# Kernel tuning notes

Measured on AMD Instinct MI355X. Metric: run time of the kernel, lower is better.

## Reference

```python
import jax, jax.numpy as jnp
import numpy as np

DIM = 768
NUM_HEADS = 12
HEAD_DIM = DIM // NUM_HEADS
H = W = 64
RANK = 4
LORA_SCALING = 1.0 / RANK  # lora_alpha(=1) / r


def setup_inputs() -> dict:
    key = jax.random.key(0)
    ks = jax.random.split(key, 11)
    s = 0.02
    return {
        "x": jax.random.normal(ks[0], (1, H, W, DIM), dtype=jnp.float32),
        "W_qkv": jax.random.normal(ks[1], (3 * DIM, DIM), dtype=jnp.float32) * s,
        "b_qkv": jax.random.normal(ks[2], (3 * DIM,), dtype=jnp.float32) * s,
        "A_q": jax.random.normal(ks[3], (RANK, DIM), dtype=jnp.float32) * s,
        "B_q": jax.random.normal(ks[4], (DIM, RANK), dtype=jnp.float32) * s,
        "A_v": jax.random.normal(ks[5], (RANK, DIM), dtype=jnp.float32) * s,
        "B_v": jax.random.normal(ks[6], (DIM, RANK), dtype=jnp.float32) * s,
        "rel_h": jax.random.normal(ks[7], (2 * H - 1, HEAD_DIM), dtype=jnp.float32) * s,
        "rel_w": jax.random.normal(ks[8], (2 * W - 1, HEAD_DIM), dtype=jnp.float32) * s,
        "W_proj": jax.random.normal(ks[9], (DIM, DIM), dtype=jnp.float32) * s,
        "b_proj": jax.random.normal(ks[10], (DIM,), dtype=jnp.float32) * s,
    }


def _get_rel_pos(size, rel_pos):
    # q_size == k_size == size; relative coords indexed into (2*size-1, head_dim)
    coords = jnp.arange(size)[:, None] - jnp.arange(size)[None, :] + (size - 1)
    return rel_pos[coords]  # (size, size, head_dim)


def reference(x, W_qkv, b_qkv, A_q, B_q, A_v, B_v, rel_h, rel_w, W_proj, b_proj):
    B, h, w, dim = x.shape
    nh, hd = NUM_HEADS, HEAD_DIM
    scale = hd ** -0.5
    n = h * w
    xf = x.reshape(B, n, dim)

    # LoRA-merged QKV: base linear + low-rank deltas on q and v thirds only
    qkv = xf @ W_qkv.T + b_qkv  # (B, n, 3*dim)
    dq = ((xf @ A_q.T) @ B_q.T) * LORA_SCALING
    dv = ((xf @ A_v.T) @ B_v.T) * LORA_SCALING
    qkv = qkv.at[..., :dim].add(dq).at[..., 2 * dim:].add(dv)

    qkv = qkv.reshape(B, n, 3, nh, hd).transpose(2, 0, 3, 1, 4).reshape(3, B * nh, n, hd)
    q, k, v = qkv[0], qkv[1], qkv[2]  # each (B*nh, n, hd)

    attn = (q * scale) @ jnp.swapaxes(k, -2, -1)  # (B*nh, n, n)

    # decomposed relative position bias (SAM style)
    Rh = _get_rel_pos(h, rel_h)  # (h, h, hd)
    Rw = _get_rel_pos(w, rel_w)  # (w, w, hd)
    r_q = q.reshape(B * nh, h, w, hd)
    bias_h = jnp.einsum("bhwc,hkc->bhwk", r_q, Rh)  # (B*nh, h, w, h)
    bias_w = jnp.einsum("bhwc,wkc->bhwk", r_q, Rw)  # (B*nh, h, w, w)
    attn = (attn.reshape(B * nh, h, w, h, w)
            + bias_h[:, :, :, :, None]
            + bias_w[:, :, :, None, :]).reshape(B * nh, n, n)

    attn = jax.nn.softmax(attn, axis=-1)
    out = (attn @ v).reshape(B, nh, h, w, hd).transpose(0, 2, 3, 1, 4).reshape(B, h, w, dim)
    return out @ W_proj.T + b_proj
```

## Files before the change

kernel.cpp:

```cpp
#include <hip/hip_runtime.h>

#define NTOK 4096
#define DIMD 768
#define NHD  12
#define HDD  64
#define DK   800

typedef float  f32x4  __attribute__((ext_vector_type(4)));
typedef float  f32x16 __attribute__((ext_vector_type(16)));
typedef short  s16x8  __attribute__((ext_vector_type(8)));

#define MFMA16(a, b, c) __builtin_amdgcn_mfma_f32_16x16x32_bf16(a, b, c, 0, 0, 0)
#define MFMA32(a, b, c) __builtin_amdgcn_mfma_f32_32x32x16_bf16(a, b, c, 0, 0, 0)

__device__ inline short f2b(float f) {
  unsigned u = __float_as_uint(f);
  u += 0x7FFFu + ((u >> 16) & 1u);
  return (short)(u >> 16);
}
__device__ inline float b2f(short s) {
  return __uint_as_float(((unsigned)(unsigned short)s) << 16);
}
__device__ inline void gl_lds16(const short* g, short* l) {
  __builtin_amdgcn_global_load_lds(
      (const __attribute__((address_space(1))) unsigned int*)g,
      (__attribute__((address_space(3))) unsigned int*)l, 16, 0, 0);
}


__global__ __launch_bounds__(64)
void k_prep_w(const float* __restrict__ Wqkv, const float* __restrict__ Bq,
              const float* __restrict__ Bv, const float* __restrict__ Wp,
              short* __restrict__ we, short* __restrict__ wpb) {
  const int j = blockIdx.x;
  const int l = threadIdx.x;
  if (j < 2304) {
#pragma unroll
    for (int k = 0; k < 12; ++k)
      we[(size_t)j * DK + l + 64 * k] = f2b(Wqkv[(size_t)j * DIMD + l + 64 * k]);
    if (l < 32) {
      int c = 768 + l;
      short v = 0;
      if (l < 4) {
        if (j < 768) v = f2b(Bq[j * 4 + l]);
      } else if (l < 8) {
        if (j >= 1536) v = f2b(Bv[(j - 1536) * 4 + (l - 4)]);
      }
      we[(size_t)j * DK + c] = v;
    }
  } else {
    const int jr = j - 2304;
#pragma unroll
    for (int k = 0; k < 12; ++k)
      wpb[(size_t)jr * DIMD + l + 64 * k] =
          f2b(Wp[(size_t)jr * DIMD + l + 64 * k]);
  }
}

__global__ __launch_bounds__(64)
void k_prep_x(const float* __restrict__ x, const float* __restrict__ Aq,
              const float* __restrict__ Av, short* __restrict__ xe) {
  const int i = blockIdx.x;
  const int l = threadIdx.x;
  float xv[12];
#pragma unroll
  for (int k = 0; k < 12; ++k) xv[k] = x[(size_t)i * DIMD + l + 64 * k];
#pragma unroll
  for (int k = 0; k < 12; ++k)
    xe[(size_t)i * DK + l + 64 * k] = f2b(xv[k]);
  float a8[8];
#pragma unroll
  for (int o = 0; o < 8; ++o) {
    const float* A = (o < 4) ? (Aq + o * DIMD) : (Av + (o - 4) * DIMD);
    float acc = 0.f;
#pragma unroll
    for (int k = 0; k < 12; ++k) acc = fmaf(xv[k], A[l + 64 * k], acc);
#pragma unroll
    for (int off = 32; off; off >>= 1) acc += __shfl_xor(acc, off, 64);
    a8[o] = acc;
  }
  if (l < 32) {
    float v = 0.f;
#pragma unroll
    for (int o = 0; o < 8; ++o)
      if (l == o) v = 0.25f * a8[o];
    xe[(size_t)i * DK + 768 + l] = (l < 8) ? f2b(v) : (short)0;
  }
}

__global__ __launch_bounds__(256)
void k_qkv(const short* __restrict__ xe, const short* __restrict__ we,
           const float* __restrict__ bqkv, short* __restrict__ qkvb) {
  const int j0 = blockIdx.x * 128;
  const int i0 = blockIdx.y * 128;
  __shared__ short As[128 * 32];
  __shared__ short Bs[128 * 32];
  __shared__ short Cs[128 * 130];
  const int t = threadIdx.x, lane = t & 63, w = t >> 6;
  const int l15 = lane & 15, quad = lane >> 4;
  const int wm = w >> 1, wn = w & 1;

  f32x4 acc[4][4];
#pragma unroll
  for (int a = 0; a < 4; ++a)
#pragma unroll
    for (int b = 0; b < 4; ++b) acc[a][b] = (f32x4){0.f, 0.f, 0.f, 0.f};

  for (int kk = 0; kk < DK; kk += 32) {
    __syncthreads();
#pragma unroll
    for (int rep = 0; rep < 2; ++rep) {
      int c = rep * 256 + w * 64 + lane;
      gl_lds16(xe + (size_t)(i0 + (c >> 2)) * DK + kk + (c & 3) * 8,
               &As[(rep * 256 + w * 64) * 8]);
      gl_lds16(we + (size_t)(j0 + (c >> 2)) * DK + kk + (c & 3) * 8,
               &Bs[(rep * 256 + w * 64) * 8]);
    }
    __syncthreads();
    s16x8 af[4], bf[4];
#pragma unroll
    for (int mt = 0; mt < 4; ++mt)
      af[mt] = *(const s16x8*)&As[(wm * 64 + mt * 16 + l15) * 32 + quad * 8];
#pragma unroll
    for (int nt = 0; nt < 4; ++nt)
      bf[nt] = *(const s16x8*)&Bs[(wn * 64 + nt * 16 + l15) * 32 + quad * 8];
#pragma unroll
    for (int mt = 0; mt < 4; ++mt)
#pragma unroll
      for (int nt = 0; nt < 4; ++nt)
        acc[mt][nt] = MFMA16(af[mt], bf[nt], acc[mt][nt]);
  }

  const int which = j0 / DIMD;
  float bj[4];
#pragma unroll
  for (int nt = 0; nt < 4; ++nt) bj[nt] = bqkv[j0 + wn * 64 + nt * 16 + l15];

#pragma unroll
  for (int mt = 0; mt < 4; ++mt)
#pragma unroll
    for (int r = 0; r < 4; ++r) {
      const int row = wm * 64 + mt * 16 + quad * 4 + r;
#pragma unroll
      for (int nt = 0; nt < 4; ++nt) {
        const int col = wn * 64 + nt * 16 + l15;
        Cs[row * 130 + col] = f2b(acc[mt][nt][r] + bj[nt]);
      }
    }
  __syncthreads();
  const int base_head = (j0 - which * DIMD) >> 6;
#pragma unroll
  for (int rp = 0; rp < 8; ++rp) {
    int f = t + 256 * rp;
    int row = f >> 4, ch = f & 15;
    int head = base_head + (ch >> 3);
    int ddb = (ch & 7) * 8;
    s16x8 v = *(const s16x8*)&Cs[row * 130 + ch * 8];
    *(s16x8*)&qkvb[(((size_t)which * NHD + head) * NTOK + i0 + row) * HDD + ddb] = v;
  }
}

__global__ __launch_bounds__(256)
void k_vt(const short* __restrict__ qkvb, short* __restrict__ vtb) {
  const int head = blockIdx.y;
  const int n0 = blockIdx.x * 64;
  const short* vg = qkvb + ((size_t)(2 * NHD + head)) * NTOK * HDD;
  __shared__ short T[64][68];
  const int t = threadIdx.x;
#pragma unroll
  for (int rp = 0; rp < 4; ++rp) {
    int f = t + 256 * rp;
    int n = f >> 4, c4 = (f & 15) * 4;
    *(short4*)&T[n][c4] = *(const short4*)&vg[(size_t)(n0 + n) * HDD + c4];
  }
  __syncthreads();
#pragma unroll
  for (int rp = 0; rp < 4; ++rp) {
    int f = t + 256 * rp;
    int d = f >> 4, n4 = (f & 15) * 4;
    const int pmap[4] = {0, 2, 1, 3};
    int n4s = (n4 & 48) | (pmap[(n4 >> 2) & 3] << 2);
    short4 o;
    o.x = T[n4s + 0][d]; o.y = T[n4s + 1][d];
    o.z = T[n4s + 2][d]; o.w = T[n4s + 3][d];
    *(short4*)&vtb[((size_t)head * HDD + d) * NTOK + n0 + n4] = o;
  }
}

__global__ __launch_bounds__(256)
void k_attn6(const short* __restrict__ qkvb, const short* __restrict__ vtb,
             const float* __restrict__ relh, const float* __restrict__ relw,
             short* __restrict__ attnb) {
  const int head = blockIdx.y;
  const int hq = blockIdx.x;
  const int n0 = hq * 64;

  __shared__ short sm[20480];
  short* smb = sm;

  const short* qg  = qkvb + (size_t)(0 * NHD + head) * NTOK * HDD;
  const short* kg  = qkvb + (size_t)(1 * NHD + head) * NTOK * HDD;
  const short* vtg = vtb + (size_t)head * HDD * NTOK;

  const int t = threadIdx.x;
  const int w = t >> 6, lane = t & 63;
  const int l31 = lane & 31, h = lane >> 5;
  const int kh = w >> 1, qh = w & 1;
  const int q = qh * 32 + l31;

  const int slot = w * 64 + lane;
  const int krow = slot >> 3;
  const int kcol = ((slot & 7) ^ (krow & 7)) * 8;
  const short* gK0 = kg + (size_t)krow * HDD + kcol;
  const short* gK1 = gK0 + 32 * HDD;
  const short* gV0 = vtg + (size_t)krow * NTOK + kcol;
  const short* gV1 = gV0 + (size_t)32 * NTOK;

  s16x8 qb[4];
#pragma unroll
  for (int s = 0; s < 4; ++s)
    qb[s] = *(const s16x8*)&qg[(size_t)(n0 + q) * HDD + s * 16 + 8 * h];

#pragma unroll
  for (int rp = 0; rp < 4; ++rp) {
    int f = t + 256 * rp;
    int d = f >> 3, c = (f & 7) * 8;
    float4 v0 = make_float4(0, 0, 0, 0), v1 = v0;
    if (d < 127) {
      const float* s_ = relw + (size_t)d * HDD + c;
      v0 = *(const float4*)s_; v1 = *(const float4*)(s_ + 4);
    }
    short4 b0, b1;
    b0.x = f2b(v0.x); b0.y = f2b(v0.y); b0.z = f2b(v0.z); b0.w = f2b(v0.w);
    b1.x = f2b(v1.x); b1.y = f2b(v1.y); b1.z = f2b(v1.z); b1.w = f2b(v1.w);
    *(short4*)&smb[d * 72 + c] = b0;
    *(short4*)&smb[d * 72 + c + 4] = b1;
  }
  __syncthreads();

  f32x16 mc0 = (f32x16)(0.f), mc1 = (f32x16)(0.f);
#pragma unroll
  for (int s = 0; s < 4; ++s) {
    s16x8 a0 = *(const s16x8*)&smb[((kh * 2) * 32 + l31) * 72 + s * 16 + 8 * h];
    s16x8 a1 = *(const s16x8*)&smb[((kh * 2 + 1) * 32 + l31) * 72 + s * 16 + 8 * h];
    mc0 = MFMA32(a0, qb[s], mc0);
    mc1 = MFMA32(a1, qb[s], mc1);
  }
  __syncthreads();
#pragma unroll
  for (int reg = 0; reg < 16; ++reg) {
    int dl = (reg & 3) + 8 * (reg >> 2) + 4 * h;
    smb[(kh * 64 + dl) * 64 + q] = f2b(mc0[reg] * 1.44269504f);
    smb[(kh * 64 + 32 + dl) * 64 + q] = f2b(mc1[reg] * 1.44269504f);
  }
  __syncthreads();

  float bwl2[16];
#pragma unroll
  for (int reg = 0; reg < 16; ++reg) {
    int kl64 = kh * 32 + (reg & 3) + 8 * (reg >> 2) + 4 * h;
    int dneed = q - kl64 + 63;
    bwl2[reg] = b2f(smb[dneed * 64 + q]);
  }
  __syncthreads();

#pragma unroll
  for (int rp = 0; rp < 2; ++rp) {
    int f = t + 256 * rp;
    int kt = f >> 3, c = (f & 7) * 8;
    const float* s_ = relh + (size_t)(hq + 63 - kt) * HDD + c;
    float4 v0 = *(const float4*)s_, v1 = *(const float4*)(s_ + 4);
    short4 b0, b1;
    b0.x = f2b(v0.x); b0.y = f2b(v0.y); b0.z = f2b(v0.z); b0.w = f2b(v0.w);
    b1.x = f2b(v1.x); b1.y = f2b(v1.y); b1.z = f2b(v1.z); b1.w = f2b(v1.w);
    *(short4*)&smb[kt * 72 + c] = b0;
    *(short4*)&smb[kt * 72 + c + 4] = b1;
  }
  __syncthreads();

  f32x16 hc = (f32x16)(0.f);
#pragma unroll
  for (int s = 0; s < 4; ++s) {
    s16x8 a = *(const s16x8*)&smb[(kh * 32 + l31) * 72 + s * 16 + 8 * h];
    hc = MFMA32(a, qb[s], hc);
  }
#pragma unroll
  for (int reg = 0; reg < 16; ++reg) {
    int ktl = kh * 32 + (reg & 3) + 8 * (reg >> 2) + 4 * h;
    smb[16384 + ktl * 64 + q] = f2b(hc[reg] * 1.44269504f);
  }
  __syncthreads();

  gl_lds16(gK0, smb + 0 + w * 512);
  gl_lds16(gK1, smb + 2048 + w * 512);
  gl_lds16(gV0, smb + 8192 + w * 512);
  gl_lds16(gV1, smb + 8192 + 2048 + w * 512);
  gK0 += 4096; gK1 += 4096;
  gV0 += 64; gV1 += 64;

  int baseS[4], baseV[2];
#pragma unroll
  for (int s = 0; s < 4; ++s)
    baseS[s] = (kh * 32 + l31) * 64 + (((2 * s + h) ^ (l31 & 7)) * 8);
#pragma unroll
  for (int s2 = 0; s2 < 2; ++s2)
    baseV[s2] = l31 * 64 + (((kh * 4 + s2 * 2 + h) ^ (l31 & 7)) * 8);

  float ps = 0.f;
  f32x16 oc0 = (f32x16)(0.f), oc1 = (f32x16)(0.f);

#define ATTN_ITER(KT, KSRC, VSRC, KDST, VDST)                                  \
  {                                                                            \
    __syncthreads();                                                           \
    if ((KT) < 63) {                                                           \
      gl_lds16(gK0, smb + (KDST) + w * 512);                                   \
      gl_lds16(gK1, smb + (KDST) + 2048 + w * 512);                            \
      gl_lds16(gV0, smb + (VDST) + w * 512);                                   \
      gl_lds16(gV1, smb + (VDST) + 2048 + w * 512);                            \
      gK0 += 4096; gK1 += 4096; gV0 += 64; gV1 += 64;                          \
    }                                                                          \
    f32x16 sc_ = (f32x16)(0.f);                                                \
    _Pragma("unroll") for (int s = 0; s < 4; ++s) {                            \
      s16x8 a = *(const s16x8*)&smb[(KSRC) + baseS[s]];                        \
      sc_ = MFMA32(a, qb[s], sc_);                                             \
    }                                                                          \
    float bhl2 = b2f(smb[16384 + (KT) * 64 + q]);                              \
    float sv[16];                                                              \
    _Pragma("unroll") for (int reg = 0; reg < 16; ++reg) {                     \
      sv[reg] = exp2f(fmaf(0.18033688f, sc_[reg], bhl2 + bwl2[reg]));          \
      ps += sv[reg];                                                           \
    }                                                                          \
    unsigned pk[8];                                                            \
    _Pragma("unroll") for (int i = 0; i < 8; ++i) {                            \
      int rl = 2 * i;                                                          \
      pk[i] = __builtin_amdgcn_perm(__float_as_uint(sv[rl + 1]),               \
                                    __float_as_uint(sv[rl]), 0x07060302u);     \
    }                                                                          \
    _Pragma("unroll") for (int s2 = 0; s2 < 2; ++s2) {                         \
      union { unsigned u[4]; s16x8 v; } B;                                     \
      B.u[0] = pk[4 * s2 + 0];                                                 \
      B.u[1] = pk[4 * s2 + 1];                                                 \
      B.u[2] = pk[4 * s2 + 2];                                                 \
      B.u[3] = pk[4 * s2 + 3];                                                 \
      s16x8 a0 = *(const s16x8*)&smb[(VSRC) + baseV[s2]];                      \
      s16x8 a1 = *(const s16x8*)&smb[(VSRC) + 2048 + baseV[s2]];               \
      oc0 = MFMA32(a0, B.v, oc0);                                              \
      oc1 = MFMA32(a1, B.v, oc1);                                              \
    }                                                                          \
  }

  for (int k2 = 0; k2 < 32; ++k2) {
    ATTN_ITER(2 * k2,     0,    8192,  4096, 12288);
    ATTN_ITER(2 * k2 + 1, 4096, 12288, 0,    8192);
  }
#undef ATTN_ITER

  __syncthreads();
  float* obuf = (float*)smb;
  float* psb  = (float*)smb + 4224;
  short* tbuf = smb + 8576;
  ps += __shfl_xor(ps, 32, 64);
  if (kh == 1) {
#pragma unroll
    for (int reg = 0; reg < 16; ++reg) {
      int dl = (reg & 3) + 8 * (reg >> 2) + 4 * h;
      obuf[dl * 66 + q] = oc0[reg];
      obuf[(32 + dl) * 66 + q] = oc1[reg];
    }
    if (lane < 32) psb[q] = ps;
  }
  __syncthreads();
  if (kh == 0) {
    float inv = 1.f / (ps + psb[q]);
#pragma unroll
    for (int reg = 0; reg < 16; ++reg) {
      int dl = (reg & 3) + 8 * (reg >> 2) + 4 * h;
      tbuf[dl * 66 + q] = f2b((oc0[reg] + obuf[dl * 66 + q]) * inv);
      tbuf[(32 + dl) * 66 + q] = f2b((oc1[reg] + obuf[(32 + dl) * 66 + q]) * inv);
    }
  }
  __syncthreads();
  {
    int qq = t >> 2, seg = t & 3;
    unsigned wds[8];
#pragma unroll
    for (int m = 0; m < 8; ++m) {
      unsigned lo = (unsigned short)tbuf[(seg * 16 + 2 * m) * 66 + qq];
      unsigned hi = (unsigned short)tbuf[(seg * 16 + 2 * m + 1) * 66 + qq];
      wds[m] = lo | (hi << 16);
    }
    short* dst = attnb + (size_t)(n0 + qq) * DIMD + head * 64 + seg * 16;
    *(int4*)dst = *(int4*)&wds[0];
    *(int4*)(dst + 8) = *(int4*)&wds[4];
  }
}

__global__ __launch_bounds__(256)
void k_proj(const short* __restrict__ ab, const short* __restrict__ wpb,
            const float* __restrict__ bp, float* __restrict__ out) {
  const int j0 = blockIdx.x * 64;
  const int i0 = blockIdx.y * 128;
  __shared__ short As[128 * 32];
  __shared__ short Bs[64 * 32];
  const int t = threadIdx.x, lane = t & 63, w = t >> 6;
  const int l15 = lane & 15, quad = lane >> 4;
  const int wm = w >> 1, wn = w & 1;

  f32x4 acc[4][2];
#pragma unroll
  for (int a = 0; a < 4; ++a)
#pragma unroll
    for (int b = 0; b < 2; ++b) acc[a][b] = (f32x4){0.f, 0.f, 0.f, 0.f};

  for (int kk = 0; kk < DIMD; kk += 32) {
    __syncthreads();
#pragma unroll
    for (int rep = 0; rep < 2; ++rep) {
      int c = rep * 256 + w * 64 + lane;
      gl_lds16(ab + (size_t)(i0 + (c >> 2)) * DIMD + kk + (c & 3) * 8,
               &As[(rep * 256 + w * 64) * 8]);
    }
    {
      gl_lds16(wpb + (size_t)(j0 + ((w * 64 + lane) >> 2)) * DIMD + kk +
                   ((w * 64 + lane) & 3) * 8,
               &Bs[(w * 64) * 8]);
    }
    __syncthreads();
    s16x8 af[4], bf[2];
#pragma unroll
    for (int mt = 0; mt < 4; ++mt)
      af[mt] = *(const s16x8*)&As[(wm * 64 + mt * 16 + l15) * 32 + quad * 8];
#pragma unroll
    for (int nt = 0; nt < 2; ++nt)
      bf[nt] = *(const s16x8*)&Bs[(wn * 32 + nt * 16 + l15) * 32 + quad * 8];
#pragma unroll
    for (int mt = 0; mt < 4; ++mt)
#pragma unroll
      for (int nt = 0; nt < 2; ++nt)
        acc[mt][nt] = MFMA16(af[mt], bf[nt], acc[mt][nt]);
  }

#pragma unroll
  for (int mt = 0; mt < 4; ++mt)
#pragma unroll
    for (int r = 0; r < 4; ++r) {
      const int i = i0 + wm * 64 + mt * 16 + quad * 4 + r;
#pragma unroll
      for (int nt = 0; nt < 2; ++nt) {
        const int j = j0 + wn * 32 + nt * 16 + l15;
        out[(size_t)i * DIMD + j] = acc[mt][nt][r] + bp[j];
      }
    }
}

extern "C" void kernel_launch(void* const* d_in, const int* in_sizes, int n_in,
                              void* d_out, int out_size, void* d_ws, size_t ws_size,
                              hipStream_t stream) {
  (void)in_sizes; (void)n_in; (void)out_size; (void)ws_size;
  const float* x    = (const float*)d_in[0];
  const float* Wqkv = (const float*)d_in[1];
  const float* bqkv = (const float*)d_in[2];
  const float* Aq   = (const float*)d_in[3];
  const float* Bq   = (const float*)d_in[4];
  const float* Av   = (const float*)d_in[5];
  const float* Bv   = (const float*)d_in[6];
  const float* relh = (const float*)d_in[7];
  const float* relw = (const float*)d_in[8];
  const float* Wp   = (const float*)d_in[9];
  const float* bp   = (const float*)d_in[10];
  float* out = (float*)d_out;

  float* ws = (float*)d_ws;
  short* xe    = (short*)(ws);
  short* we    = (short*)(ws + 1638400);
  short* wpb   = (short*)(ws + 2560000);
  short* qkvb  = (short*)(ws + 2854912);
  short* vtb   = (short*)(ws + 7573504);
  short* attnb = (short*)(ws + 9146368);

  k_prep_w<<<dim3(3072), dim3(64), 0, stream>>>(Wqkv, Bq, Bv, Wp, we, wpb);
  k_prep_x<<<dim3(NTOK), dim3(64), 0, stream>>>(x, Aq, Av, xe);
  k_qkv<<<dim3(18, 32), dim3(256), 0, stream>>>(xe, we, bqkv, qkvb);
  k_vt<<<dim3(64, NHD), dim3(256), 0, stream>>>(qkvb, vtb);
  k_attn6<<<dim3(64, NHD), dim3(256), 0, stream>>>(qkvb, vtb, relh, relw, attnb);
  k_proj<<<dim3(12, 32), dim3(256), 0, stream>>>(attnb, wpb, bp, out);
}
```

Before: 242.8 us.

## Fuse V transpose into QKV epilogue and vectorize softmax exp with packed math

The QKV GEMM epilogue now writes the V third straight out in transposed, permuted layout from its shared-memory tile, so the separate k_vt kernel launch and its extra global round trip go away. The attention kernel also computes the scaled-logit-plus-bias step on two-element float vectors, which allows packed FMA, and uses the hardware exp2 builtin in place of exp2f. In exchange, the V epilogue does strided 16-bit LDS reads, and the builtin exp2 may handle denormals less precisely.

```diff
diff --git a/kernel.cpp b/kernel.cpp
--- a/kernel.cpp
+++ b/kernel.cpp
@@ -6,12 +6,19 @@
 #define HDD  64
 #define DK   800
 
+typedef float  f32x2  __attribute__((ext_vector_type(2)));
 typedef float  f32x4  __attribute__((ext_vector_type(4)));
 typedef float  f32x16 __attribute__((ext_vector_type(16)));
 typedef short  s16x8  __attribute__((ext_vector_type(8)));
 
 #define MFMA16(a, b, c) __builtin_amdgcn_mfma_f32_16x16x32_bf16(a, b, c, 0, 0, 0)
 #define MFMA32(a, b, c) __builtin_amdgcn_mfma_f32_32x32x16_bf16(a, b, c, 0, 0, 0)
+
+#if __has_builtin(__builtin_amdgcn_exp2f)
+#define EXP2(x) __builtin_amdgcn_exp2f(x)
+#else
+#define EXP2(x) exp2f(x)
+#endif
 
 __device__ inline short f2b(float f) {
   unsigned u = __float_as_uint(f);
@@ -90,7 +97,8 @@
 
 __global__ __launch_bounds__(256)
 void k_qkv(const short* __restrict__ xe, const short* __restrict__ we,
-           const float* __restrict__ bqkv, short* __restrict__ qkvb) {
+           const float* __restrict__ bqkv, short* __restrict__ qkvb,
+           short* __restrict__ vtb) {
   const int j0 = blockIdx.x * 128;
   const int i0 = blockIdx.y * 128;
   __shared__ short As[128 * 32];
@@ -149,46 +157,39 @@
     }
   __syncthreads();
   const int base_head = (j0 - which * DIMD) >> 6;
-#pragma unroll
-  for (int rp = 0; rp < 8; ++rp) {
-    int f = t + 256 * rp;
-    int row = f >> 4, ch = f & 15;
-    int head = base_head + (ch >> 3);
-    int ddb = (ch & 7) * 8;
-    s16x8 v = *(const s16x8*)&Cs[row * 130 + ch * 8];
-    *(s16x8*)&qkvb[(((size_t)which * NHD + head) * NTOK + i0 + row) * HDD + ddb] = v;
+  if (which != 2) {
+#pragma unroll
+    for (int rp = 0; rp < 8; ++rp) {
+      int f = t + 256 * rp;
+      int row = f >> 4, ch = f & 15;
+      int head = base_head + (ch >> 3);
+      int ddb = (ch & 7) * 8;
+      s16x8 v = *(const s16x8*)&Cs[row * 130 + ch * 8];
+      *(s16x8*)&qkvb[(((size_t)which * NHD + head) * NTOK + i0 + row) * HDD + ddb] = v;
+    }
+  } else {
+#pragma unroll
+    for (int rp = 0; rp < 8; ++rp) {
+      int f = t + 256 * rp;
+      int dcol = f >> 4, n8 = (f & 15) * 8;
+      unsigned wds[4];
+#pragma unroll
+      for (int m = 0; m < 4; ++m) {
+        int s0 = n8 + 2 * m, s1 = s0 + 1;
+        int sr0 = (s0 & 0x70) | ((((s0 >> 2) & 3) == 1 ? 2 : ((s0 >> 2) & 3) == 2 ? 1 : ((s0 >> 2) & 3)) << 2) | (s0 & 3);
+        int sr1 = (s1 & 0x70) | ((((s1 >> 2) & 3) == 1 ? 2 : ((s1 >> 2) & 3) == 2 ? 1 : ((s1 >> 2) & 3)) << 2) | (s1 & 3);
+        unsigned lo = (unsigned short)Cs[sr0 * 130 + dcol];
+        unsigned hi = (unsigned short)Cs[sr1 * 130 + dcol];
+        wds[m] = lo | (hi << 16);
+      }
+      short* dst = vtb + ((size_t)(base_head * 64) + dcol) * NTOK + i0 + n8;
+      *(int4*)dst = *(int4*)&wds[0];
+    }
   }
 }
 
 __global__ __launch_bounds__(256)
-void k_vt(const short* __restrict__ qkvb, short* __restrict__ vtb) {
-  const int head = blockIdx.y;
-  const int n0 = blockIdx.x * 64;
-  const short* vg = qkvb + ((size_t)(2 * NHD + head)) * NTOK * HDD;
-  __shared__ short T[64][68];
-  const int t = threadIdx.x;
-#pragma unroll
-  for (int rp = 0; rp < 4; ++rp) {
-    int f = t + 256 * rp;
-    int n = f >> 4, c4 = (f & 15) * 4;
-    *(short4*)&T[n][c4] = *(const short4*)&vg[(size_t)(n0 + n) * HDD + c4];
-  }
-  __syncthreads();
-#pragma unroll
-  for (int rp = 0; rp < 4; ++rp) {
-    int f = t + 256 * rp;
-    int d = f >> 4, n4 = (f & 15) * 4;
-    const int pmap[4] = {0, 2, 1, 3};
-    int n4s = (n4 & 48) | (pmap[(n4 >> 2) & 3] << 2);
-    short4 o;
-    o.x = T[n4s + 0][d]; o.y = T[n4s + 1][d];
-    o.z = T[n4s + 2][d]; o.w = T[n4s + 3][d];
-    *(short4*)&vtb[((size_t)head * HDD + d) * NTOK + n0 + n4] = o;
-  }
-}
-
-__global__ __launch_bounds__(256)
-void k_attn6(const short* __restrict__ qkvb, const short* __restrict__ vtb,
+void k_attn7(const short* __restrict__ qkvb, const short* __restrict__ vtb,
              const float* __restrict__ relh, const float* __restrict__ relw,
              short* __restrict__ attnb) {
   const int head = blockIdx.y;
@@ -255,13 +256,16 @@
   }
   __syncthreads();
 
-  float bwl2[16];
-#pragma unroll
-  for (int reg = 0; reg < 16; ++reg) {
-    int kl64 = kh * 32 + (reg & 3) + 8 * (reg >> 2) + 4 * h;
-    int dneed = q - kl64 + 63;
-    bwl2[reg] = b2f(smb[dneed * 64 + q]);
-  }
+  f32x2 bw2[8];
+#pragma unroll
+  for (int i = 0; i < 8; ++i)
+#pragma unroll
+    for (int p = 0; p < 2; ++p) {
+      int reg = 2 * i + p;
+      int kl64 = kh * 32 + (reg & 3) + 8 * (reg >> 2) + 4 * h;
+      int dneed = q - kl64 + 63;
+      bw2[i][p] = b2f(smb[dneed * 64 + q]);
+    }
   __syncthreads();
 
 #pragma unroll
@@ -306,7 +310,7 @@
   for (int s2 = 0; s2 < 2; ++s2)
     baseV[s2] = l31 * 64 + (((kh * 4 + s2 * 2 + h) ^ (l31 & 7)) * 8);
 
-  float ps = 0.f;
+  f32x2 ps2 = (f32x2)(0.f);
   f32x16 oc0 = (f32x16)(0.f), oc1 = (f32x16)(0.f);
 
 #define ATTN_ITER(KT, KSRC, VSRC, KDST, VDST)                                  \
@@ -325,25 +329,26 @@
       sc_ = MFMA32(a, qb[s], sc_);                                             \
     }                                                                          \
     float bhl2 = b2f(smb[16384 + (KT) * 64 + q]);                              \
-    float sv[16];                                                              \
-    _Pragma("unroll") for (int reg = 0; reg < 16; ++reg) {                     \
-      sv[reg] = exp2f(fmaf(0.18033688f, sc_[reg], bhl2 + bwl2[reg]));          \
-      ps += sv[reg];                                                           \
-    }                                                                          \
     unsigned pk[8];                                                            \
     _Pragma("unroll") for (int i = 0; i < 8; ++i) {                            \
-      int rl = 2 * i;                                                          \
-      pk[i] = __builtin_amdgcn_perm(__float_as_uint(sv[rl + 1]),               \
-                                    __float_as_uint(sv[rl]), 0x07060302u);     \
+      f32x2 s2;                                                                \
+      s2[0] = sc_[2 * i]; s2[1] = sc_[2 * i + 1];                              \
+      f32x2 r = s2 * 0.18033688f + (bw2[i] + bhl2);                            \
+      float e0 = EXP2(r[0]);                                                   \
+      float e1 = EXP2(r[1]);                                                   \
+      f32x2 e2; e2[0] = e0; e2[1] = e1;                                        \
+      ps2 += e2;                                                               \
+      pk[i] = __builtin_amdgcn_perm(__float_as_uint(e1),                       \
+                                    __float_as_uint(e0), 0x07060302u);         \
     }                                                                          \
-    _Pragma("unroll") for (int s2 = 0; s2 < 2; ++s2) {                         \
+    _Pragma("unroll") for (int s2i = 0; s2i < 2; ++s2i) {                      \
       union { unsigned u[4]; s16x8 v; } B;                                     \
-      B.u[0] = pk[4 * s2 + 0];                                                 \
-      B.u[1] = pk[4 * s2 + 1];                                                 \
-      B.u[2] = pk[4 * s2 + 2];                                                 \
-      B.u[3] = pk[4 * s2 + 3];                                                 \
-      s16x8 a0 = *(const s16x8*)&smb[(VSRC) + baseV[s2]];                      \
-      s16x8 a1 = *(const s16x8*)&smb[(VSRC) + 2048 + baseV[s2]];               \
+      B.u[0] = pk[4 * s2i + 0];                                                \
+      B.u[1] = pk[4 * s2i + 1];                                                \
+      B.u[2] = pk[4 * s2i + 2];                                                \
+      B.u[3] = pk[4 * s2i + 3];                                                \
+      s16x8 a0 = *(const s16x8*)&smb[(VSRC) + baseV[s2i]];                     \
+      s16x8 a1 = *(const s16x8*)&smb[(VSRC) + 2048 + baseV[s2i]];              \
       oc0 = MFMA32(a0, B.v, oc0);                                              \
       oc1 = MFMA32(a1, B.v, oc1);                                              \
     }                                                                          \
@@ -356,6 +361,7 @@
 #undef ATTN_ITER
 
   __syncthreads();
+  float ps = ps2[0] + ps2[1];
   float* obuf = (float*)smb;
   float* psb  = (float*)smb + 4224;
   short* tbuf = smb + 8576;
@@ -480,8 +486,7 @@
 
   k_prep_w<<<dim3(3072), dim3(64), 0, stream>>>(Wqkv, Bq, Bv, Wp, we, wpb);
   k_prep_x<<<dim3(NTOK), dim3(64), 0, stream>>>(x, Aq, Av, xe);
-  k_qkv<<<dim3(18, 32), dim3(256), 0, stream>>>(xe, we, bqkv, qkvb);
-  k_vt<<<dim3(64, NHD), dim3(256), 0, stream>>>(qkvb, vtb);
-  k_attn6<<<dim3(64, NHD), dim3(256), 0, stream>>>(qkvb, vtb, relh, relw, attnb);
+  k_qkv<<<dim3(18, 32), dim3(256), 0, stream>>>(xe, we, bqkv, qkvb, vtb);
+  k_attn7<<<dim3(64, NHD), dim3(256), 0, stream>>>(qkvb, vtb, relh, relw, attnb);
   k_proj<<<dim3(12, 32), dim3(256), 0, stream>>>(attnb, wpb, bp, out);
 }
```

Result: faster. 220.4 us (-9.2%).
